# Optimization experiments

Measured on AMD Instinct MI355X. Metric: run time of the kernel, lower is better.

Reference implementation:

```python
import jax, jax.numpy as jnp
import numpy as np
import math

LOG2 = math.log(2.0)

def shifted_softplus(x):
    return jax.nn.softplus(x) - LOG2

def setup_inputs() -> dict:
    key = jax.random.key(0)
    ks = jax.random.split(key, 12)
    n_atoms, n_pairs = 40000, 640000
    d_basis, d_filt, n_rbf = 128, 128, 20
    x = jax.random.normal(ks[0], (n_atoms, d_basis), dtype=jnp.float32)
    f_ij = jax.random.uniform(ks[1], (n_pairs, n_rbf), dtype=jnp.float32)
    idx_i = jax.random.randint(ks[2], (n_pairs,), 0, n_atoms)
    idx_j = jax.random.randint(ks[3], (n_pairs,), 0, n_atoms)
    rcut_ij = jax.random.uniform(ks[4], (n_pairs,), dtype=jnp.float32)
    s_in = 1.0 / math.sqrt(d_basis)
    s_f = 1.0 / math.sqrt(n_rbf)
    s_out = 1.0 / math.sqrt(d_filt)
    W_in = jax.random.uniform(ks[5], (d_filt, d_basis), minval=-s_in, maxval=s_in)
    b_in = jax.random.uniform(ks[6], (d_filt,), minval=-s_in, maxval=s_in)
    W_f = jax.random.uniform(ks[7], (d_filt, n_rbf), minval=-s_f, maxval=s_f)
    b_f = jax.random.uniform(ks[8], (d_filt,), minval=-s_f, maxval=s_f)
    W_out = jax.random.uniform(ks[9], (d_basis, d_filt), minval=-s_out, maxval=s_out)
    b_out = jax.random.uniform(ks[10], (d_basis,), minval=-s_out, maxval=s_out)
    return {"x": x, "f_ij": f_ij, "idx_i": idx_i, "idx_j": idx_j, "rcut_ij": rcut_ij,
            "W_in": W_in, "b_in": b_in, "W_f": W_f, "b_f": b_f, "W_out": W_out, "b_out": b_out}

def reference(x, f_ij, idx_i, idx_j, rcut_ij, W_in, b_in, W_f, b_f, W_out, b_out):
    n_atoms = x.shape[0]
    # input_to_feature: Linear(d_basis -> d_filt)
    h = x @ W_in.T + b_in                                  # [n_atoms, d_filt]
    # filter_network: Linear(n_rbf -> d_filt) + ShiftedSoftplus, scaled by cutoff
    Wij = shifted_softplus(f_ij @ W_f.T + b_f) * rcut_ij[:, None]  # [n_pairs, d_filt]
    # gather neighbor features, modulate, scatter-add back to atoms
    x_ij = h[idx_j] * Wij                                  # [n_pairs, d_filt]
    agg = jax.ops.segment_sum(x_ij, idx_i, num_segments=n_atoms)   # [n_atoms, d_filt]
    # feature_to_output: Linear(d_filt -> d_basis) + ShiftedSoftplus
    return shifted_softplus(agg @ W_out.T + b_out)
```

## Files before the change

kernel.cpp:

```cpp
#include <hip/hip_runtime.h>
#include <hip/hip_bf16.h>
#include <hip/hip_fp16.h>

typedef __hip_bfloat16 bf16;
typedef __attribute__((ext_vector_type(8))) short short8;
typedef __attribute__((ext_vector_type(4))) float f32x4;
typedef __attribute__((ext_vector_type(2))) _Float16 h16x2;

#if defined(__has_builtin)
#if __has_builtin(__builtin_amdgcn_fdot2)
#define HAVE_FDOT2 1
#endif
#endif

__device__ __forceinline__ float braw2f(unsigned short u) {
    return __uint_as_float(((unsigned int)u) << 16);
}
__device__ __forceinline__ unsigned short f2braw(float f) {
    bf16 b = __float2bfloat16(f);
    return *(unsigned short*)&b;
}
__device__ __forceinline__ unsigned int pack2(float lo, float hi) {
    return (unsigned int)f2braw(lo) | ((unsigned int)f2braw(hi) << 16);
}
__device__ __forceinline__ unsigned int pack2h(float lo, float hi) {
    __half l = __float2half(lo), h = __float2half(hi);
    return (unsigned int)*(unsigned short*)&l | ((unsigned int)*(unsigned short*)&h << 16);
}
__device__ __forceinline__ float fdot2(h16x2 a, h16x2 b, float c) {
#ifdef HAVE_FDOT2
    return __builtin_amdgcn_fdot2(a, b, c, false);
#else
    return c + (float)a[0] * (float)b[0] + (float)a[1] * (float)b[1];
#endif
}
__device__ __forceinline__ h16x2 u2h2(unsigned int u) {
    union { unsigned int u; h16x2 h; } cv; cv.u = u; return cv.h;
}

#define LN2F 0.69314718055994531f
__device__ __forceinline__ float ssp(float x) {
    return fmaxf(x, 0.0f) + __logf(1.0f + __expf(-fabsf(x))) - LN2F;
}

template<bool ACT, bool OUT_BF16>
__global__ __launch_bounds__(256) void linear128_mfma_kernel(
    const float* __restrict__ X, const float* __restrict__ W, const float* __restrict__ Bias,
    void* __restrict__ Yv, int n_rows)
{
    __shared__ unsigned short wls[128 * 128];
    __shared__ unsigned short xs[64 * 128];
    __shared__ float bls[128];

    const float4* W4 = (const float4*)W;
    for (int i = threadIdx.x; i < 128 * 32; i += 256) {
        float4 w = W4[i];
        ushort4 s; s.x = f2braw(w.x); s.y = f2braw(w.y); s.z = f2braw(w.z); s.w = f2braw(w.w);
        *(ushort4*)&wls[i * 4] = s;
    }
    if (threadIdx.x < 128) bls[threadIdx.x] = Bias[threadIdx.x];

    const int base = blockIdx.x * 64;
    const float4* X4 = (const float4*)X;
    for (int i = threadIdx.x; i < 64 * 32; i += 256) {
        int r = i >> 5, k4 = i & 31;
        int row = base + r;
        float4 v = (row < n_rows) ? X4[(size_t)row * 32 + k4] : make_float4(0.f, 0.f, 0.f, 0.f);
        ushort4 s; s.x = f2braw(v.x); s.y = f2braw(v.y); s.z = f2braw(v.z); s.w = f2braw(v.w);
        *(ushort4*)&xs[r * 128 + k4 * 4] = s;
    }
    __syncthreads();

    const int wv = threadIdx.x >> 6;
    const int l  = threadIdx.x & 63;
    const int lm = l & 15;
    const int lq = l >> 4;

    short8 a[4];
    #pragma unroll
    for (int kk = 0; kk < 4; ++kk)
        a[kk] = *(const short8*)&xs[(wv * 16 + lm) * 128 + kk * 32 + lq * 8];

    f32x4 acc[8];
    #pragma unroll
    for (int ct = 0; ct < 8; ++ct) {
        f32x4 c = {0.f, 0.f, 0.f, 0.f};
        #pragma unroll
        for (int kk = 0; kk < 4; ++kk) {
            short8 b = *(const short8*)&wls[(ct * 16 + lm) * 128 + kk * 32 + lq * 8];
            c = __builtin_amdgcn_mfma_f32_16x16x32_bf16(a[kk], b, c, 0, 0, 0);
        }
        acc[ct] = c;
    }

    #pragma unroll
    for (int ct = 0; ct < 8; ++ct) {
        int col = ct * 16 + lm;
        float bia = bls[col];
        #pragma unroll
        for (int r = 0; r < 4; ++r) {
            int row = base + wv * 16 + lq * 4 + r;
            if (row < n_rows) {
                float o = acc[ct][r] + bia;
                if (ACT) o = ssp(o);
                if (OUT_BF16) ((unsigned short*)Yv)[(size_t)row * 128 + col] = f2braw(o);
                else          ((float*)Yv)[(size_t)row * 128 + col] = o;
            }
        }
    }
}


__global__ __launch_bounds__(256) void zero_int_kernel(int* __restrict__ p, int n) {
    int i = blockIdx.x * 256 + threadIdx.x;
    if (i < n) p[i] = 0;
}

__global__ __launch_bounds__(256) void hist_kernel(
    const int* __restrict__ idx_i, int* __restrict__ cnt, int n_pairs, int n_atoms)
{
    for (int p = blockIdx.x * 256 + threadIdx.x; p < n_pairs; p += gridDim.x * 256) {
        int ai = idx_i[p];
        if ((unsigned)ai < (unsigned)n_atoms) atomicAdd(&cnt[ai], 1);
    }
}

__global__ __launch_bounds__(1024) void scan1_kernel(
    const int* __restrict__ cnt, int* __restrict__ offs, int* __restrict__ partials, int n)
{
    __shared__ int sm[1024];
    int t = threadIdx.x, idx = blockIdx.x * 1024 + t;
    int v = (idx < n) ? cnt[idx] : 0;
    sm[t] = v;
    __syncthreads();
    #pragma unroll
    for (int d = 1; d < 1024; d <<= 1) {
        int tmp = (t >= d) ? sm[t - d] : 0;
        __syncthreads();
        sm[t] += tmp;
        __syncthreads();
    }
    if (idx < n) offs[idx] = sm[t] - v;
    if (t == 1023) partials[blockIdx.x] = sm[1023];
}

__global__ __launch_bounds__(64) void scan2_kernel(
    int* __restrict__ partials, int* __restrict__ offs, int nb, int n)
{
    __shared__ int sm[64];
    int t = threadIdx.x;
    int v = (t < nb) ? partials[t] : 0;
    sm[t] = v;
    __syncthreads();
    #pragma unroll
    for (int d = 1; d < 64; d <<= 1) {
        int tmp = (t >= d) ? sm[t - d] : 0;
        __syncthreads();
        sm[t] += tmp;
        __syncthreads();
    }
    if (t < nb) partials[t] = sm[t] - v;
    if (t == 63) offs[n] = sm[63];
}

__global__ __launch_bounds__(1024) void scan3_kernel(
    int* __restrict__ offs, int* __restrict__ cur, const int* __restrict__ partials, int n)
{
    int idx = blockIdx.x * 1024 + threadIdx.x;
    if (idx < n) {
        int o = offs[idx] + partials[blockIdx.x];
        offs[idx] = o;
        cur[idx] = o;
    }
}

__global__ __launch_bounds__(256) void scatter_pay_kernel(
    const float* __restrict__ f_ij, const int* __restrict__ idx_i, const int* __restrict__ idx_j,
    const float* __restrict__ rcut, int* __restrict__ cur, uint4* __restrict__ pay,
    int n_pairs, int n_atoms)
{
    if (blockIdx.x == 0 && threadIdx.x < 204) {
        ((int*)(pay + (size_t)n_pairs * 3))[threadIdx.x] = 0;
    }
    for (int p = blockIdx.x * 256 + threadIdx.x; p < n_pairs; p += gridDim.x * 256) {
        int ai = idx_i[p];
        if ((unsigned)ai >= (unsigned)n_atoms) continue;
        int pos = atomicAdd(&cur[ai], 1);
        const float4* fr = (const float4*)(f_ij + (size_t)p * 20);
        float4 f0 = fr[0], f1 = fr[1], f2 = fr[2], f3 = fr[3], f4 = fr[4];
        uint4 q0, q1, q2;
        q0.x = pack2h(f0.x, f0.y); q0.y = pack2h(f0.z, f0.w);
        q0.z = pack2h(f1.x, f1.y); q0.w = pack2h(f1.z, f1.w);
        q1.x = pack2h(f2.x, f2.y); q1.y = pack2h(f2.z, f2.w);
        q1.z = pack2h(f3.x, f3.y); q1.w = pack2h(f3.z, f3.w);
        q2.x = pack2h(f4.x, f4.y); q2.y = pack2h(f4.z, f4.w);
        q2.z = (unsigned int)idx_j[p];
        q2.w = __float_as_uint(rcut[p]);
        uint4* dst = pay + (size_t)pos * 3;
        dst[0] = q0; dst[1] = q1; dst[2] = q2;
    }
}

__global__ __launch_bounds__(256) void segment_pay_f16_kernel(
    const uint4* __restrict__ pay, const float* __restrict__ W_f,
    const float* __restrict__ b_f, const unsigned int* __restrict__ hb32,
    const int* __restrict__ offs, float* __restrict__ agg, int n_atoms)
{
    const int wave = (blockIdx.x * 256 + threadIdx.x) >> 6;
    const int lane = threadIdx.x & 63;
    if (wave >= n_atoms) return;

    const int c0 = 2 * lane;
    float wt[40];
    {
        const float4* wf4 = (const float4*)(W_f + (size_t)c0 * 20);
        #pragma unroll
        for (int r = 0; r < 10; ++r) {
            float4 v = wf4[r];
            wt[4 * r + 0] = v.x; wt[4 * r + 1] = v.y;
            wt[4 * r + 2] = v.z; wt[4 * r + 3] = v.w;
        }
    }
    h16x2 w0p[10], w1p[10];
    #pragma unroll
    for (int r = 0; r < 10; ++r) {
        h16x2 a, b;
        a[0] = (_Float16)wt[2 * r];
        a[1] = (_Float16)wt[2 * r + 1];
        b[0] = (_Float16)wt[20 + 2 * r];
        b[1] = (_Float16)wt[20 + 2 * r + 1];
        w0p[r] = a; w1p[r] = b;
    }
    const float b0 = b_f[c0], b1 = b_f[c0 + 1];

    const int cs = __builtin_amdgcn_readfirstlane(offs[wave]);
    const int ce = __builtin_amdgcn_readfirstlane(offs[wave + 1]);
    float acc0 = 0.f, acc1 = 0.f;

    int s = cs;
    for (; s + 2 <= ce; s += 2) {
        const uint4* pA = pay + (size_t)s * 3;
        const uint4* pB = pA + 3;
        uint4 qA0 = pA[0], qA1 = pA[1], qA2 = pA[2];
        uint4 qB0 = pB[0], qB1 = pB[1], qB2 = pB[2];
        unsigned int uA[10] = {qA0.x,qA0.y,qA0.z,qA0.w,qA1.x,qA1.y,qA1.z,qA1.w,qA2.x,qA2.y};
        unsigned int uB[10] = {qB0.x,qB0.y,qB0.z,qB0.w,qB1.x,qB1.y,qB1.z,qB1.w,qB2.x,qB2.y};
        float a0A = b0, a1A = b1, a0B = b0, a1B = b1;
        #pragma unroll
        for (int r = 0; r < 10; ++r) {
            h16x2 fA = u2h2(uA[r]);
            h16x2 fB = u2h2(uB[r]);
            a0A = fdot2(fA, w0p[r], a0A);
            a1A = fdot2(fA, w1p[r], a1A);
            a0B = fdot2(fB, w0p[r], a0B);
            a1B = fdot2(fB, w1p[r], a1B);
        }
        float rcA = __uint_as_float(qA2.w), rcB = __uint_as_float(qB2.w);
        float wv0A = ssp(a0A) * rcA, wv1A = ssp(a1A) * rcA;
        float wv0B = ssp(a0B) * rcB, wv1B = ssp(a1B) * rcB;
        unsigned int hA = hb32[(size_t)(int)qA2.z * 64 + lane];
        unsigned int hB = hb32[(size_t)(int)qB2.z * 64 + lane];
        acc0 += __uint_as_float(hA << 16) * wv0A + __uint_as_float(hB << 16) * wv0B;
        acc1 += __uint_as_float(hA & 0xffff0000u) * wv1A + __uint_as_float(hB & 0xffff0000u) * wv1B;
    }
    if (s < ce) {
        const uint4* pA = pay + (size_t)s * 3;
        uint4 q0 = pA[0], q1 = pA[1], q2 = pA[2];
        unsigned int u[10] = {q0.x,q0.y,q0.z,q0.w,q1.x,q1.y,q1.z,q1.w,q2.x,q2.y};
        float a0 = b0, a1 = b1;
        #pragma unroll
        for (int r = 0; r < 10; ++r) {
            h16x2 f = u2h2(u[r]);
            a0 = fdot2(f, w0p[r], a0);
            a1 = fdot2(f, w1p[r], a1);
        }
        float rc = __uint_as_float(q2.w);
        float wv0 = ssp(a0) * rc, wv1 = ssp(a1) * rc;
        unsigned int h = hb32[(size_t)(int)q2.z * 64 + lane];
        acc0 += __uint_as_float(h << 16) * wv0;
        acc1 += __uint_as_float(h & 0xffff0000u) * wv1;
    }

    *(float2*)&agg[(size_t)wave * 128 + c0] = make_float2(acc0, acc1);
}

__global__ __launch_bounds__(256) void scatter_kernel(
    const int* __restrict__ idx_i, int* __restrict__ cur, int* __restrict__ perm,
    int n_pairs, int n_atoms)
{
    for (int p = blockIdx.x * 256 + threadIdx.x; p < n_pairs; p += gridDim.x * 256) {
        int ai = idx_i[p];
        if ((unsigned)ai < (unsigned)n_atoms) {
            int pos = atomicAdd(&cur[ai], 1);
            perm[pos] = p;
        }
    }
}

__global__ __launch_bounds__(256) void segment_kernel(
    const float* __restrict__ f_ij, const int* __restrict__ idx_j,
    const float* __restrict__ rcut, const float* __restrict__ W_f,
    const float* __restrict__ b_f, const unsigned short* __restrict__ hb,
    const int* __restrict__ offs, const int* __restrict__ perm,
    float* __restrict__ agg, int n_atoms)
{
    const int wave = (blockIdx.x * 256 + threadIdx.x) >> 6;
    const int lane = threadIdx.x & 63;
    if (wave >= n_atoms) return;

    float w0[20], w1[20];
    #pragma unroll
    for (int r = 0; r < 20; ++r) {
        w0[r] = W_f[lane * 20 + r];
        w1[r] = W_f[(lane + 64) * 20 + r];
    }
    const float b0 = b_f[lane], b1 = b_f[lane + 64];

    const int cs = offs[wave], ce = offs[wave + 1];
    float acc0 = 0.f, acc1 = 0.f;

    int s = cs;
    for (; s + 2 <= ce; s += 2) {
        int pA = perm[s], pB = perm[s + 1];
        int ajA = idx_j[pA], ajB = idx_j[pB];
        float rcA = rcut[pA], rcB = rcut[pB];
        const float4* frA = (const float4*)(f_ij + (size_t)pA * 20);
        const float4* frB = (const float4*)(f_ij + (size_t)pB * 20);
        float a0A = b0, a1A = b1, a0B = b0, a1B = b1;
        #pragma unroll
        for (int q = 0; q < 5; ++q) {
            float4 fA = frA[q], fB = frB[q];
            a0A += fA.x * w0[4*q+0]; a1A += fA.x * w1[4*q+0];
            a0A += fA.y * w0[4*q+1]; a1A += fA.y * w1[4*q+1];
            a0A += fA.z * w0[4*q+2]; a1A += fA.z * w1[4*q+2];
            a0A += fA.w * w0[4*q+3]; a1A += fA.w * w1[4*q+3];
            a0B += fB.x * w0[4*q+0]; a1B += fB.x * w1[4*q+0];
            a0B += fB.y * w0[4*q+1]; a1B += fB.y * w1[4*q+1];
            a0B += fB.z * w0[4*q+2]; a1B += fB.z * w1[4*q+2];
            a0B += fB.w * w0[4*q+3]; a1B += fB.w * w1[4*q+3];
        }
        float wv0A = ssp(a0A) * rcA, wv1A = ssp(a1A) * rcA;
        float wv0B = ssp(a0B) * rcB, wv1B = ssp(a1B) * rcB;
        float h0A = braw2f(hb[(size_t)ajA * 128 + lane]);
        float h1A = braw2f(hb[(size_t)ajA * 128 + 64 + lane]);
        float h0B = braw2f(hb[(size_t)ajB * 128 + lane]);
        float h1B = braw2f(hb[(size_t)ajB * 128 + 64 + lane]);
        acc0 += h0A * wv0A + h0B * wv0B;
        acc1 += h1A * wv1A + h1B * wv1B;
    }
    if (s < ce) {
        int p = perm[s];
        int aj = idx_j[p];
        float rc = rcut[p];
        const float4* fr = (const float4*)(f_ij + (size_t)p * 20);
        float a0 = b0, a1 = b1;
        #pragma unroll
        for (int q = 0; q < 5; ++q) {
            float4 fv = fr[q];
            a0 += fv.x * w0[4*q+0]; a1 += fv.x * w1[4*q+0];
            a0 += fv.y * w0[4*q+1]; a1 += fv.y * w1[4*q+1];
            a0 += fv.z * w0[4*q+2]; a1 += fv.z * w1[4*q+2];
            a0 += fv.w * w0[4*q+3]; a1 += fv.w * w1[4*q+3];
        }
        float wv0 = ssp(a0) * rc, wv1 = ssp(a1) * rc;
        acc0 += braw2f(hb[(size_t)aj * 128 + lane]) * wv0;
        acc1 += braw2f(hb[(size_t)aj * 128 + 64 + lane]) * wv1;
    }

    agg[(size_t)wave * 128 + lane]      = acc0;
    agg[(size_t)wave * 128 + 64 + lane] = acc1;
}

static inline size_t align_up(size_t v, size_t a) { return (v + a - 1) & ~(a - 1); }

extern "C" void kernel_launch(void* const* d_in, const int* in_sizes, int n_in,
                              void* d_out, int out_size, void* d_ws, size_t ws_size,
                              hipStream_t stream) {
    const float* x     = (const float*)d_in[0];
    const float* f_ij  = (const float*)d_in[1];
    const int*   idx_i = (const int*)d_in[2];
    const int*   idx_j = (const int*)d_in[3];
    const float* rcut  = (const float*)d_in[4];
    const float* W_in  = (const float*)d_in[5];
    const float* b_in  = (const float*)d_in[6];
    const float* W_f   = (const float*)d_in[7];
    const float* b_f   = (const float*)d_in[8];
    const float* W_out = (const float*)d_in[9];
    const float* b_out = (const float*)d_in[10];

    const int n_atoms = in_sizes[0] / 128;
    const int n_pairs = in_sizes[2];
    const int nscan = (n_atoms + 1023) / 1024;
    const int mfma_grid = (n_atoms + 63) / 64;

    size_t off_hb   = 0;
    size_t off_offs = align_up(off_hb + (size_t)n_atoms * 128 * 2, 16);
    size_t off_cur  = align_up(off_offs + (size_t)(n_atoms + 1) * 4, 16);
    size_t off_part = align_up(off_cur + (size_t)n_atoms * 4, 16);
    size_t off_pay  = align_up(off_part + (size_t)nscan * 4, 64);
    size_t need_pay = off_pay + (size_t)n_pairs * 48 + 816;

    if (ws_size >= need_pay) {
        unsigned short* hb = (unsigned short*)((char*)d_ws + off_hb);
        int*  offs = (int*)((char*)d_ws + off_offs);
        int*  cur  = (int*)((char*)d_ws + off_cur);
        int*  part = (int*)((char*)d_ws + off_part);
        uint4* pay = (uint4*)((char*)d_ws + off_pay);
        float* agg = (float*)d_out;

        linear128_mfma_kernel<false, true><<<dim3(mfma_grid), dim3(256), 0, stream>>>(
            x, W_in, b_in, (void*)hb, n_atoms);

        zero_int_kernel<<<dim3((n_atoms + 255) / 256), dim3(256), 0, stream>>>(cur, n_atoms);
        hist_kernel<<<dim3(1024), dim3(256), 0, stream>>>(idx_i, cur, n_pairs, n_atoms);
        scan1_kernel<<<dim3(nscan), dim3(1024), 0, stream>>>(cur, offs, part, n_atoms);
        scan2_kernel<<<dim3(1), dim3(64), 0, stream>>>(part, offs, nscan, n_atoms);
        scan3_kernel<<<dim3(nscan), dim3(1024), 0, stream>>>(offs, cur, part, n_atoms);
        scatter_pay_kernel<<<dim3(1024), dim3(256), 0, stream>>>(
            f_ij, idx_i, idx_j, rcut, cur, pay, n_pairs, n_atoms);

        segment_pay_f16_kernel<<<dim3((n_atoms + 3) / 4), dim3(256), 0, stream>>>(
            pay, W_f, b_f, (const unsigned int*)hb, offs, agg, n_atoms);

        linear128_mfma_kernel<true, false><<<dim3(mfma_grid), dim3(256), 0, stream>>>(
            agg, W_out, b_out, d_out, n_atoms);
    } else {
        size_t o_h    = 0;
        size_t o_offs = o_h + (size_t)n_atoms * 128 * 2;
        size_t o_cur  = o_offs + (size_t)(n_atoms + 1) * 4;
        size_t o_perm = o_cur + (size_t)n_atoms * 4;
        size_t o_part = o_perm + (size_t)n_pairs * 4;
        unsigned short* hb = (unsigned short*)((char*)d_ws + o_h);
        int* offs = (int*)((char*)d_ws + o_offs);
        int* cur  = (int*)((char*)d_ws + o_cur);
        int* perm = (int*)((char*)d_ws + o_perm);
        int* part = (int*)((char*)d_ws + o_part);
        float* agg = (float*)d_out;

        linear128_mfma_kernel<false, true><<<dim3(mfma_grid), dim3(256), 0, stream>>>(
            x, W_in, b_in, (void*)hb, n_atoms);

        zero_int_kernel<<<dim3((n_atoms + 255) / 256), dim3(256), 0, stream>>>(cur, n_atoms);
        hist_kernel<<<dim3(1024), dim3(256), 0, stream>>>(idx_i, cur, n_pairs, n_atoms);
        scan1_kernel<<<dim3(nscan), dim3(1024), 0, stream>>>(cur, offs, part, n_atoms);
        scan2_kernel<<<dim3(1), dim3(64), 0, stream>>>(part, offs, nscan, n_atoms);
        scan3_kernel<<<dim3(nscan), dim3(1024), 0, stream>>>(offs, cur, part, n_atoms);
        scatter_kernel<<<dim3(1024), dim3(256), 0, stream>>>(idx_i, cur, perm, n_pairs, n_atoms);

        segment_kernel<<<dim3((n_atoms + 3) / 4), dim3(256), 0, stream>>>(
            f_ij, idx_j, rcut, W_f, b_f, hb, offs, perm, agg, n_atoms);

        linear128_mfma_kernel<true, false><<<dim3(mfma_grid), dim3(256), 0, stream>>>(
            agg, W_out, b_out, d_out, n_atoms);
    }
}
```

Baseline: 316.9 us.

## Fuse counting-sort pipeline into one cooperative kernel with grid syncs

Replaces six separate launches (zero, histogram, three-pass scan, payload scatter) with one cooperative kernel that uses grid-wide syncs between phases. The scan is redone with 256-element chunks and a single-block second level. The goal is to remove per-launch overhead and the idle gaps between small kernels. In exchange it adds grid.sync barriers and depends on all 1024 blocks being co-resident, and it also zeroes a small tail region of the payload.

```diff
diff --git a/kernel.cpp b/kernel.cpp
--- a/kernel.cpp
+++ b/kernel.cpp
@@ -1,6 +1,9 @@
 #include <hip/hip_runtime.h>
 #include <hip/hip_bf16.h>
 #include <hip/hip_fp16.h>
+#include <hip/hip_cooperative_groups.h>
+
+namespace cg = cooperative_groups;
 
 typedef __hip_bfloat16 bf16;
 typedef __attribute__((ext_vector_type(8))) short short8;
@@ -19,9 +22,6 @@
 __device__ __forceinline__ unsigned short f2braw(float f) {
     bf16 b = __float2bfloat16(f);
     return *(unsigned short*)&b;
-}
-__device__ __forceinline__ unsigned int pack2(float lo, float hi) {
-    return (unsigned int)f2braw(lo) | ((unsigned int)f2braw(hi) << 16);
 }
 __device__ __forceinline__ unsigned int pack2h(float lo, float hi) {
     __half l = __float2half(lo), h = __float2half(hi);
@@ -107,6 +107,88 @@
                 else          ((float*)Yv)[(size_t)row * 128 + col] = o;
             }
         }
+    }
+}
+
+__global__ __launch_bounds__(256) void coop_sort_kernel(
+    const float* __restrict__ f_ij, const int* __restrict__ idx_i,
+    const int* __restrict__ idx_j, const float* __restrict__ rcut,
+    int* __restrict__ cur, int* __restrict__ offs, int* __restrict__ part,
+    uint4* __restrict__ pay, int n_pairs, int n_atoms)
+{
+    cg::grid_group grid = cg::this_grid();
+    __shared__ int sm[256];
+    const int tid = blockIdx.x * 256 + threadIdx.x;
+    const int nth = gridDim.x * 256;
+    const int nchunk = (n_atoms + 255) / 256;
+
+    for (int i = tid; i < n_atoms; i += nth) cur[i] = 0;
+    if (tid < 204) ((int*)(pay + (size_t)n_pairs * 3))[tid] = 0;
+    grid.sync();
+
+    for (int p = tid; p < n_pairs; p += nth) {
+        int ai = idx_i[p];
+        if ((unsigned)ai < (unsigned)n_atoms) atomicAdd(&cur[ai], 1);
+    }
+    grid.sync();
+
+    for (int c = blockIdx.x; c < nchunk; c += gridDim.x) {
+        int idx = c * 256 + threadIdx.x;
+        int v = (idx < n_atoms) ? cur[idx] : 0;
+        sm[threadIdx.x] = v;
+        __syncthreads();
+        #pragma unroll
+        for (int d = 1; d < 256; d <<= 1) {
+            int tmp = (threadIdx.x >= d) ? sm[threadIdx.x - d] : 0;
+            __syncthreads();
+            sm[threadIdx.x] += tmp;
+            __syncthreads();
+        }
+        if (idx < n_atoms) offs[idx] = sm[threadIdx.x] - v;
+        if (threadIdx.x == 255) part[c] = sm[255];
+        __syncthreads();
+    }
+    grid.sync();
+
+    if (blockIdx.x == 0) {
+        int v = (threadIdx.x < nchunk) ? part[threadIdx.x] : 0;
+        sm[threadIdx.x] = v;
+        __syncthreads();
+        #pragma unroll
+        for (int d = 1; d < 256; d <<= 1) {
+            int tmp = (threadIdx.x >= d) ? sm[threadIdx.x - d] : 0;
+            __syncthreads();
+            sm[threadIdx.x] += tmp;
+            __syncthreads();
+        }
+        if (threadIdx.x < nchunk) part[threadIdx.x] = sm[threadIdx.x] - v;
+        if (threadIdx.x == 255) offs[n_atoms] = sm[255];
+    }
+    grid.sync();
+
+    for (int i = tid; i < n_atoms; i += nth) {
+        int o = offs[i] + part[i >> 8];
+        offs[i] = o;
+        cur[i] = o;
+    }
+    grid.sync();
+
+    for (int p = tid; p < n_pairs; p += nth) {
+        int ai = idx_i[p];
+        if ((unsigned)ai >= (unsigned)n_atoms) continue;
+        int pos = atomicAdd(&cur[ai], 1);
+        const float4* fr = (const float4*)(f_ij + (size_t)p * 20);
+        float4 f0 = fr[0], f1 = fr[1], f2 = fr[2], f3 = fr[3], f4 = fr[4];
+        uint4 q0, q1, q2;
+        q0.x = pack2h(f0.x, f0.y); q0.y = pack2h(f0.z, f0.w);
+        q0.z = pack2h(f1.x, f1.y); q0.w = pack2h(f1.z, f1.w);
+        q1.x = pack2h(f2.x, f2.y); q1.y = pack2h(f2.z, f2.w);
+        q1.z = pack2h(f3.x, f3.y); q1.w = pack2h(f3.z, f3.w);
+        q2.x = pack2h(f4.x, f4.y); q2.y = pack2h(f4.z, f4.w);
+        q2.z = (unsigned int)idx_j[p];
+        q2.w = __float_as_uint(rcut[p]);
+        uint4* dst = pay + (size_t)pos * 3;
+        dst[0] = q0; dst[1] = q1; dst[2] = q2;
     }
 }
 
@@ -391,13 +473,14 @@
     const int n_atoms = in_sizes[0] / 128;
     const int n_pairs = in_sizes[2];
     const int nscan = (n_atoms + 1023) / 1024;
+    const int nchunk = (n_atoms + 255) / 256;
     const int mfma_grid = (n_atoms + 63) / 64;
 
     size_t off_hb   = 0;
     size_t off_offs = align_up(off_hb + (size_t)n_atoms * 128 * 2, 16);
     size_t off_cur  = align_up(off_offs + (size_t)(n_atoms + 1) * 4, 16);
     size_t off_part = align_up(off_cur + (size_t)n_atoms * 4, 16);
-    size_t off_pay  = align_up(off_part + (size_t)nscan * 4, 64);
+    size_t off_pay  = align_up(off_part + (size_t)(nchunk + 64) * 4, 64);
     size_t need_pay = off_pay + (size_t)n_pairs * 48 + 816;
 
     if (ws_size >= need_pay) {
@@ -411,13 +494,24 @@
         linear128_mfma_kernel<false, true><<<dim3(mfma_grid), dim3(256), 0, stream>>>(
             x, W_in, b_in, (void*)hb, n_atoms);
 
-        zero_int_kernel<<<dim3((n_atoms + 255) / 256), dim3(256), 0, stream>>>(cur, n_atoms);
-        hist_kernel<<<dim3(1024), dim3(256), 0, stream>>>(idx_i, cur, n_pairs, n_atoms);
-        scan1_kernel<<<dim3(nscan), dim3(1024), 0, stream>>>(cur, offs, part, n_atoms);
-        scan2_kernel<<<dim3(1), dim3(64), 0, stream>>>(part, offs, nscan, n_atoms);
-        scan3_kernel<<<dim3(nscan), dim3(1024), 0, stream>>>(offs, cur, part, n_atoms);
-        scatter_pay_kernel<<<dim3(1024), dim3(256), 0, stream>>>(
-            f_ij, idx_i, idx_j, rcut, cur, pay, n_pairs, n_atoms);
+        if (nchunk <= 256) {
+            int np = n_pairs, na = n_atoms;
+            void* cargs[] = {
+                (void*)&f_ij, (void*)&idx_i, (void*)&idx_j, (void*)&rcut,
+                (void*)&cur, (void*)&offs, (void*)&part, (void*)&pay,
+                (void*)&np, (void*)&na
+            };
+            hipLaunchCooperativeKernel((const void*)coop_sort_kernel,
+                                       dim3(1024), dim3(256), cargs, 0, stream);
+        } else {
+            zero_int_kernel<<<dim3((n_atoms + 255) / 256), dim3(256), 0, stream>>>(cur, n_atoms);
+            hist_kernel<<<dim3(1024), dim3(256), 0, stream>>>(idx_i, cur, n_pairs, n_atoms);
+            scan1_kernel<<<dim3(nscan), dim3(1024), 0, stream>>>(cur, offs, part, n_atoms);
+            scan2_kernel<<<dim3(1), dim3(64), 0, stream>>>(part, offs, nscan, n_atoms);
+            scan3_kernel<<<dim3(nscan), dim3(1024), 0, stream>>>(offs, cur, part, n_atoms);
+            scatter_pay_kernel<<<dim3(1024), dim3(256), 0, stream>>>(
+                f_ij, idx_i, idx_j, rcut, cur, pay, n_pairs, n_atoms);
+        }
 
         segment_pay_f16_kernel<<<dim3((n_atoms + 3) / 4), dim3(256), 0, stream>>>(
             pay, W_f, b_f, (const unsigned int*)hb, offs, agg, n_atoms);
```

Result: slower. 789.1 us (+149.0%).
